# Performance work log

Hardware: AMD Instinct MI355X
Metric: run time of the kernel (lower is better)

The kernel has to match this reference:

```python
import jax, jax.numpy as jnp
from jax import lax
import numpy as np

K_SIZE = 3  # deformable kernel size
PAD = 1
STRIDE = 1


def _conv3x3(x, w, b):
    # plain 3x3 conv, pad 1, stride 1, NCHW/OIHW
    y = lax.conv_general_dilated(x, w, window_strides=(1, 1),
                                 padding=[(1, 1), (1, 1)],
                                 dimension_numbers=('NCHW', 'OIHW', 'NCHW'))
    return y + b[None, :, None, None]


def _deform_sample(x, py, px):
    """Bilinear sample x [B,C,H,W] at float coords py,px [B,K,Ho,Wo].
    Out-of-bounds samples contribute zero (matches torchvision deform_conv2d).
    Returns [B,C,K,Ho,Wo]."""
    B, C, H, W = x.shape
    y0 = jnp.floor(py)
    x0 = jnp.floor(px)
    gat = jax.vmap(lambda img, iy, ix: img[:, iy, ix])  # per-batch gather -> [C,K,Ho,Wo]
    out = jnp.zeros((B, C) + py.shape[1:], dtype=x.dtype)
    for yc, xc in ((y0, x0), (y0, x0 + 1), (y0 + 1, x0), (y0 + 1, x0 + 1)):
        wgt = (1.0 - jnp.abs(py - yc)) * (1.0 - jnp.abs(px - xc))
        valid = (yc >= 0) & (yc <= H - 1) & (xc >= 0) & (xc <= W - 1)
        wgt = jnp.where(valid, wgt, 0.0)
        iy = jnp.clip(yc, 0, H - 1).astype(jnp.int32)
        ix = jnp.clip(xc, 0, W - 1).astype(jnp.int32)
        out = out + wgt[:, None] * gat(x, iy, ix)
    return out


def reference(x, w_off, b_off, w_mask, b_mask, w_dcn, b_dcn):
    k = K_SIZE
    K = k * k
    B, C, H, W = x.shape
    # offset conv (2*K channels: (dy, dx) pairs per kernel position, row-major)
    offset = _conv3x3(x, w_off, b_off)            # [B, 2K, H, W]
    mask = jax.nn.sigmoid(_conv3x3(x, w_mask, b_mask))  # [B, K, H, W]
    off = offset.reshape(B, K, 2, H, W)
    dy, dx = off[:, :, 0], off[:, :, 1]
    ki = (jnp.arange(K) // k).astype(x.dtype)  # kernel row index
    kj = (jnp.arange(K) % k).astype(x.dtype)   # kernel col index
    # sampling coordinates: out position * stride - pad + kernel pos + learned offset
    py = (jnp.arange(H, dtype=x.dtype)[None, None, :, None] * STRIDE - PAD
          + ki[None, :, None, None] + dy)
    px = (jnp.arange(W, dtype=x.dtype)[None, None, None, :] * STRIDE - PAD
          + kj[None, :, None, None] + dx)
    val = _deform_sample(x, py, px) * mask[:, None]   # [B,C,K,H,W]
    Cout = w_dcn.shape[0]
    out = jnp.einsum('ock,bckhw->bohw', w_dcn.reshape(Cout, C, K), val)
    return out + b_dcn[None, :, None, None]


def setup_inputs() -> dict:
    key = jax.random.key(0)
    ks = jax.random.split(key, 6)
    B, C, Cout, H, W, k = 4, 256, 256, 64, 64, 3
    K = k * k
    x = jax.random.normal(ks[0], (B, C, H, W), dtype=jnp.float32)
    # NOTE: original inits offset/mask conv to zeros (degenerate -> plain conv).
    # Use small random weights so offsets/masks are nontrivial but local.
    w_off = jax.random.normal(ks[1], (2 * K, C, 3, 3), dtype=jnp.float32) * 0.01
    b_off = jnp.zeros((2 * K,), dtype=jnp.float32)
    w_mask = jax.random.normal(ks[2], (K, C, 3, 3), dtype=jnp.float32) * 0.01
    b_mask = jnp.zeros((K,), dtype=jnp.float32)
    fan_in = C * K
    w_dcn = jax.random.normal(ks[3], (Cout, C, 3, 3), dtype=jnp.float32) / np.sqrt(fan_in)
    b_dcn = jnp.zeros((Cout,), dtype=jnp.float32)
    return {"x": x, "w_off": w_off, "b_off": b_off, "w_mask": w_mask,
            "b_mask": b_mask, "w_dcn": w_dcn, "b_dcn": b_dcn}
```

## Files before the change

kernel.cpp:

```cpp
#include <hip/hip_runtime.h>
#include <math.h>

#define B_ 4
#define C_ 256
#define CO_ 256
#define H_ 64
#define W_ 64
#define HW_ 4096
#define KK_ 9
#define NCH_ 27

typedef __attribute__((ext_vector_type(8))) short bf16x8;
typedef __attribute__((ext_vector_type(4))) float f32x4;
typedef __attribute__((ext_vector_type(2))) float f32x2;

__device__ inline unsigned short f32_to_bf16(float f) {
    unsigned int u = __float_as_uint(f);
    unsigned int r = (u + 0x7FFFu + ((u >> 16) & 1u)) >> 16;
    return (unsigned short)r;
}

__global__ void prep_all(const float* __restrict__ x, unsigned short* __restrict__ xTh,
                         const float* __restrict__ w_dcn, const float* __restrict__ w_off,
                         const float* __restrict__ w_mask,
                         unsigned short* __restrict__ wTs, unsigned short* __restrict__ wCs) {
    __shared__ float tile[32][33];
    __shared__ float lw[2304];
    const int t = threadIdx.x;
    const int bid = blockIdx.x;
    if (bid < 4096) {
        const int tx = t & 31, ty = t >> 5;
        const int b = bid >> 10;
        const int rem = bid & 1023;
        const int c0 = (rem >> 7) << 5;
        const int hw0 = (rem & 127) << 5;
        const float* xb = x + ((size_t)b << 20);
        unsigned short* xTb = xTh + ((size_t)b << 20);
#pragma unroll
        for (int r = 0; r < 4; ++r) {
            int row = ty + (r << 3);
            tile[row][tx] = xb[((size_t)(c0 + row) << 12) + hw0 + tx];
        }
        __syncthreads();
#pragma unroll
        for (int r = 0; r < 4; ++r) {
            int row = ty + (r << 3);
            xTb[((size_t)(hw0 + row) << 8) + c0 + tx] = f32_to_bf16(tile[tx][row]);
        }
    } else if (bid < 4352) {
        const int o = bid - 4096;
        for (int e = t; e < 2304; e += 256) lw[e] = w_dcn[(size_t)o * 2304 + e];
        __syncthreads();
        for (int e = t; e < 2304; e += 256) {
            int k = e >> 8, c = e & 255;
            int chunk = (k << 2) + (c >> 6), ck = c & 63;
            int pos = (o << 6) + (((ck >> 3) ^ (o & 7)) << 3) + (ck & 7);
            wTs[(size_t)chunk * 16384 + pos] = f32_to_bf16(lw[c * 9 + k]);
        }
    } else {
        const int ch = bid - 4352;
        const float* src = (ch < 18) ? w_off + (size_t)ch * 2304
                         : (ch < NCH_) ? w_mask + (size_t)(ch - 18) * 2304
                         : nullptr;
        for (int e = t; e < 2304; e += 256) lw[e] = src ? src[e] : 0.f;
        __syncthreads();
        for (int e = t; e < 2304; e += 256) {
            int k = e >> 8, c = e & 255;
            int chunk = (k << 2) + (c >> 6), ck = c & 63;
            int pos = (ch << 6) + (((ck >> 3) ^ (ch & 7)) << 3) + (ck & 7);
            wCs[(size_t)chunk * 2048 + pos] = f32_to_bf16(lw[c * 9 + k]);
        }
    }
}

__global__ __launch_bounds__(256, 2) void conv_mfma(
    const unsigned short* __restrict__ xTh, const unsigned short* __restrict__ wCs,
    const float* __restrict__ b_off, const float* __restrict__ b_mask,
    float* __restrict__ offmask) {
    __shared__ alignas(16) unsigned short wlds[3][2048];
    __shared__ alignas(16) unsigned short xlds[3][2048];
    const int t = threadIdx.x;
    const int bid = blockIdx.x;
    const int b = (bid & 7) >> 1;
    const int ph = bid & 1;
    const int hh = bid >> 3;
    const unsigned short* xb = xTh + ((size_t)b << 20);

    auto stage_w = [&](int chunk, int slot) {
        const unsigned short* g = wCs + ((size_t)chunk << 11) + (t << 3);
        __builtin_amdgcn_global_load_lds(
            (const __attribute__((address_space(1))) unsigned int*)g,
            (__attribute__((address_space(3))) unsigned int*)&wlds[slot][t << 3], 16, 0, 0);
    };

    const int xp = t >> 3, xcs = t & 7;
    uint4 xr;
    bool xvalid;
    auto xload = [&](int chunk) {
        int k = chunk >> 2, cc = chunk & 3;
        int ki = k / 3, kj = k % 3;
        int py = hh + ki - 1;
        int px = (ph << 5) + xp + kj - 1;
        xvalid = (py >= 0) & (py < H_) & (px >= 0) & (px < W_);
        int pyc = min(max(py, 0), 63), pxc = min(max(px, 0), 63);
        xr = *(const uint4*)(xb + (((size_t)((pyc << 6) + pxc)) << 8) + (cc << 6) + (xcs << 3));
    };
    auto xwrite = [&](int slot) {
        uint4 u = xvalid ? xr : make_uint4(0u, 0u, 0u, 0u);
        *(uint4*)&xlds[slot][(xp << 6) + ((xcs ^ (xp & 7)) << 3)] = u;
    };

    const int wid = t >> 6, lane = t & 63;
    const int wc = wid >> 1, wp = wid & 1;
    const int m16 = lane & 15, kg = lane >> 4;
    f32x4 acc = {};

    auto compute = [&](int slot) {
#pragma unroll
        for (int ks = 0; ks < 2; ++ks) {
            int s = (ks << 2) + kg;
            int o = (wc << 4) + m16;
            bf16x8 a = *(const bf16x8*)&wlds[slot][(o << 6) + ((s ^ (o & 7)) << 3)];
            int p = (wp << 4) + m16;
            bf16x8 bf = *(const bf16x8*)&xlds[slot][(p << 6) + ((s ^ (p & 7)) << 3)];
            acc = __builtin_amdgcn_mfma_f32_16x16x32_bf16(a, bf, acc, 0, 0, 0);
        }
    };

    xload(0);
    stage_w(0, 0);
    asm volatile("s_waitcnt vmcnt(1)" ::: "memory");
    xwrite(0);

    for (int c = 0; c < 35; ++c) {
        xload(c + 1);
        stage_w(c + 1, (c + 1) % 3);
        asm volatile("s_waitcnt vmcnt(1)" ::: "memory");
        xwrite((c + 1) % 3);
        asm volatile("s_waitcnt lgkmcnt(0)" ::: "memory");
        __builtin_amdgcn_s_barrier();
        asm volatile("" ::: "memory");
        compute(c % 3);
    }
    asm volatile("s_waitcnt vmcnt(0)" ::: "memory");
    asm volatile("s_waitcnt lgkmcnt(0)" ::: "memory");
    __builtin_amdgcn_s_barrier();
    asm volatile("" ::: "memory");
    compute(35 % 3);

    const int pix = (hh << 6) + (ph << 5) + (wp << 4) + m16;
#pragma unroll
    for (int r = 0; r < 4; ++r) {
        int ch = (wc << 4) + (kg << 2) + r;
        if (ch < NCH_) {
            float bias = (ch < 18) ? b_off[ch] : b_mask[ch - 18];
            offmask[(((size_t)b * NCH_ + ch) << 12) + pix] = acc[r] + bias;
        }
    }
}

__global__ __launch_bounds__(512, 4) void dcn_fused(
    const unsigned short* __restrict__ xTh, const float* __restrict__ offmask,
    const unsigned short* __restrict__ wTs, unsigned short* __restrict__ part) {
    __shared__ ushort4 cwh[576];
    __shared__ uchar4 coffb[576];
    __shared__ alignas(16) unsigned short wbuf[2][16384];
    __shared__ alignas(16) unsigned short vbuf[4096];

    const int t = threadIdx.x;
    const int bid = blockIdx.x;
    const int b = (bid & 7) >> 1;
    const int half = bid & 1;
    const int tile64 = bid >> 3;
    const int pix0 = tile64 << 6;
    const unsigned short* xb = xTh + ((size_t)b << 20);
    const float* omb = offmask + (((size_t)b * NCH_) << 12);

    for (int e = t; e < 576; e += 512) {
        int k = e >> 6, p = e & 63;
        int pix = pix0 + p;
        int hh = pix >> 6, ww = pix & 63;
        float dy = omb[((size_t)(2 * k) << 12) + pix];
        float dx = omb[((size_t)(2 * k + 1) << 12) + pix];
        float ml = omb[((size_t)(18 + k) << 12) + pix];
        float m = 1.f / (1.f + __expf(-ml));
        float py = (float)(hh - 1 + (k / 3)) + dy;
        float px = (float)(ww - 1 + (k % 3)) + dx;
        float fy0 = floorf(py), fx0 = floorf(px);
        float ay = py - fy0, ax = px - fx0;
        bool y0v = (fy0 >= 0.f) && (fy0 <= 63.f);
        bool y1v = (fy0 >= -1.f) && (fy0 <= 62.f);
        bool x0v = (fx0 >= 0.f) && (fx0 <= 63.f);
        bool x1v = (fx0 >= -1.f) && (fx0 <= 62.f);
        int y0 = (int)fy0, x0 = (int)fx0;
        int iy0 = min(max(y0, 0), 63), iy1 = min(max(y0 + 1, 0), 63);
        int ix0 = min(max(x0, 0), 63), ix1 = min(max(x0 + 1, 0), 63);
        float w00 = (y0v && x0v) ? m * (1.f - ay) * (1.f - ax) : 0.f;
        float w01 = (y0v && x1v) ? m * (1.f - ay) * ax : 0.f;
        float w10 = (y1v && x0v) ? m * ay * (1.f - ax) : 0.f;
        float w11 = (y1v && x1v) ? m * ay * ax : 0.f;
        cwh[e] = make_ushort4(f32_to_bf16(w00), f32_to_bf16(w01),
                              f32_to_bf16(w10), f32_to_bf16(w11));
        coffb[e] = make_uchar4((unsigned char)iy0, (unsigned char)ix0,
                               (unsigned char)iy1, (unsigned char)ix1);
    }

    const int oct = t & 7, pq = t >> 3;
    const int wid = t >> 6, lane = t & 63;
    const int wo = wid >> 1, wp = wid & 1;
    const int m16 = lane & 15, kg = lane >> 4;
    const int vslot = (pq << 6) + ((oct ^ (pq & 7)) << 3);

    auto stage_w = [&](int c, int slot) {
        int gc = ((c >> 1) << 2) + (half << 1) + (c & 1);
#pragma unroll
        for (int r = 0; r < 4; ++r) {
            int off16 = (r << 9) + t;
            const unsigned short* g = wTs + ((size_t)gc << 14) + (off16 << 3);
            __builtin_amdgcn_global_load_lds(
                (const __attribute__((address_space(1))) unsigned int*)g,
                (__attribute__((address_space(3))) unsigned int*)&wbuf[slot][off16 << 3], 16, 0, 0);
        }
    };

    auto gather = [&](int c, uint4* g) {
        int k = c >> 1, cc = (half << 1) + (c & 1);
        uchar4 q = coffb[(k << 6) + pq];
        const unsigned short* cb = xb + (cc << 6) + (oct << 3);
        g[0] = *(const uint4*)(cb + ((((int)q.x << 6) + q.y) << 8));
        g[1] = *(const uint4*)(cb + ((((int)q.x << 6) + q.w) << 8));
        g[2] = *(const uint4*)(cb + ((((int)q.z << 6) + q.y) << 8));
        g[3] = *(const uint4*)(cb + ((((int)q.z << 6) + q.w) << 8));
    };

    auto finish = [&](int c, const uint4* g) {
        int k = c >> 1;
        ushort4 wv = cwh[(k << 6) + pq];
        float w0 = __uint_as_float((unsigned int)wv.x << 16);
        float w1 = __uint_as_float((unsigned int)wv.y << 16);
        float w2 = __uint_as_float((unsigned int)wv.z << 16);
        float w3 = __uint_as_float((unsigned int)wv.w << 16);
        union { uint4 v; unsigned int u[4]; } A, B2, C2, D2;
        A.v = g[0]; B2.v = g[1]; C2.v = g[2]; D2.v = g[3];
        unsigned int o4[4];
#pragma unroll
        for (int j = 0; j < 4; ++j) {
            f32x2 a2 = {__uint_as_float(A.u[j] << 16),  __uint_as_float(A.u[j] & 0xffff0000u)};
            f32x2 b2 = {__uint_as_float(B2.u[j] << 16), __uint_as_float(B2.u[j] & 0xffff0000u)};
            f32x2 c2 = {__uint_as_float(C2.u[j] << 16), __uint_as_float(C2.u[j] & 0xffff0000u)};
            f32x2 d2 = {__uint_as_float(D2.u[j] << 16), __uint_as_float(D2.u[j] & 0xffff0000u)};
            f32x2 v2 = a2 * w0 + b2 * w1 + c2 * w2 + d2 * w3;
            unsigned int pk;
            asm("v_cvt_pk_bf16_f32 %0, %1, %2" : "=v"(pk) : "v"(v2.x), "v"(v2.y));
            o4[j] = pk;
        }
        *(uint4*)&vbuf[vslot] = make_uint4(o4[0], o4[1], o4[2], o4[3]);
    };

    f32x4 acc[4][2] = {};

    auto compute = [&](int slot) {
#pragma unroll
        for (int ks = 0; ks < 2; ++ks) {
            int s = (ks << 2) + kg;
            bf16x8 aF[4], bF[2];
#pragma unroll
            for (int i = 0; i < 4; ++i) {
                int o = (wo << 6) + (i << 4) + m16;
                aF[i] = *(const bf16x8*)&wbuf[slot][(o << 6) + ((s ^ (o & 7)) << 3)];
            }
#pragma unroll
            for (int j = 0; j < 2; ++j) {
                int p = (wp << 5) + (j << 4) + m16;
                bF[j] = *(const bf16x8*)&vbuf[(p << 6) + ((s ^ (p & 7)) << 3)];
            }
#pragma unroll
            for (int i = 0; i < 4; ++i)
#pragma unroll
                for (int j = 0; j < 2; ++j)
                    acc[i][j] = __builtin_amdgcn_mfma_f32_16x16x32_bf16(
                        aF[i], bF[j], acc[i][j], 0, 0, 0);
        }
    };

    uint4 gA[4], gB[4];

    __syncthreads();
    gather(0, gA);
    stage_w(0, 0);

#define HALFSTEP(CUR, GCUR, GNXT, NW1, NW2)                              \
    __builtin_amdgcn_s_barrier();                                        \
    asm volatile("" ::: "memory");                                       \
    if ((CUR) + 1 < 18) { gather((CUR) + 1, GNXT); stage_w((CUR) + 1, ((CUR) + 1) & 1); } \
    asm volatile("s_waitcnt vmcnt(" #NW1 ")" ::: "memory");              \
    finish((CUR), GCUR);                                                 \
    asm volatile("s_waitcnt vmcnt(" #NW2 ") lgkmcnt(0)" ::: "memory");   \
    __builtin_amdgcn_s_barrier();                                        \
    asm volatile("" ::: "memory");                                       \
    __builtin_amdgcn_s_setprio(1);                                       \
    compute((CUR) & 1);                                                  \
    __builtin_amdgcn_s_setprio(0);

    for (int c = 0; c < 16; c += 2) {
        HALFSTEP(c, gA, gB, 12, 8)
        HALFSTEP(c + 1, gB, gA, 12, 8)
    }
    HALFSTEP(16, gA, gB, 12, 8)
    HALFSTEP(17, gB, gA, 4, 0)
#undef HALFSTEP

    unsigned short* pd = part + (((size_t)((half << 2) + b)) << 20);
#pragma unroll
    for (int i = 0; i < 4; ++i) {
        int ob = (wo << 6) + (i << 4) + (kg << 2);
#pragma unroll
        for (int j = 0; j < 2; ++j) {
            int p = pix0 + (wp << 5) + (j << 4) + m16;
#pragma unroll
            for (int r = 0; r < 4; ++r) {
                int oo = ob + r;
                pd[(((size_t)oo) << 12) + p] = f32_to_bf16(acc[i][j][r]);
            }
        }
    }
}

__global__ __launch_bounds__(256) void combine_out(
    const unsigned short* __restrict__ part, const float* __restrict__ b_dcn,
    float* __restrict__ out) {
    int i = (blockIdx.x * 256 + threadIdx.x) << 3;
    float bias = b_dcn[(i >> 12) & 255];
    union { uint4 v; unsigned int u[4]; } A, B2;
    A.v  = *(const uint4*)(part + i);
    B2.v = *(const uint4*)(part + ((size_t)4 << 20) + i);
    float r[8];
#pragma unroll
    for (int j = 0; j < 4; ++j) {
        float a_lo = __uint_as_float(A.u[j] << 16);
        float a_hi = __uint_as_float(A.u[j] & 0xffff0000u);
        float b_lo = __uint_as_float(B2.u[j] << 16);
        float b_hi = __uint_as_float(B2.u[j] & 0xffff0000u);
        r[2 * j]     = a_lo + b_lo + bias;
        r[2 * j + 1] = a_hi + b_hi + bias;
    }
    *(float4*)(out + i)     = make_float4(r[0], r[1], r[2], r[3]);
    *(float4*)(out + i + 4) = make_float4(r[4], r[5], r[6], r[7]);
}

extern "C" void kernel_launch(void* const* d_in, const int* in_sizes, int n_in,
                              void* d_out, int out_size, void* d_ws, size_t ws_size,
                              hipStream_t stream) {
    const float* x      = (const float*)d_in[0];
    const float* w_off  = (const float*)d_in[1];
    const float* b_off  = (const float*)d_in[2];
    const float* w_mask = (const float*)d_in[3];
    const float* b_mask = (const float*)d_in[4];
    const float* w_dcn  = (const float*)d_in[5];
    const float* b_dcn  = (const float*)d_in[6];
    float* out = (float*)d_out;

    float* ws = (float*)d_ws;
    float* offmask = ws;
    unsigned short* xTh = (unsigned short*)(offmask + (size_t)B_ * NCH_ * HW_);
    unsigned short* wTs = xTh + ((size_t)B_ * HW_ * C_);
    unsigned short* wCs = wTs + (size_t)36 * 16384;
    unsigned short* part = wCs + (size_t)36 * 2048;

    prep_all<<<dim3(4384), dim3(256), 0, stream>>>(x, xTh, w_dcn, w_off, w_mask, wTs, wCs);
    conv_mfma<<<dim3(512), dim3(256), 0, stream>>>(xTh, wCs, b_off, b_mask, offmask);
    dcn_fused<<<dim3(512), dim3(512), 0, stream>>>(xTh, offmask, wTs, part);
    combine_out<<<dim3(2048), dim3(256), 0, stream>>>(part, b_dcn, out);
}
```

Baseline: 72.87 us.

## Fuse split-K combine into DCN kernel via last-arriver atomic flags

Removes the separate combine_out launch. Each dcn_fused block increments a per-(batch,tile) atomic counter after writing its bf16 partial, and the second arriving block sums both halves, adds the bias and writes the fp32 output. Flags are zeroed in prep_all. This saves one kernel launch and a full pass over the partials, at the cost of an atomic, two extra barriers and a tail of combine work in half the blocks. Correctness depends on acquire/release ordering of the partial writes through the agent-scope atomic.

Measured after the change: 90.31 us. 23.9% more time.

```diff
diff --git a/kernel.cpp b/kernel.cpp
--- a/kernel.cpp
+++ b/kernel.cpp
@@ -23,7 +23,8 @@
 __global__ void prep_all(const float* __restrict__ x, unsigned short* __restrict__ xTh,
                          const float* __restrict__ w_dcn, const float* __restrict__ w_off,
                          const float* __restrict__ w_mask,
-                         unsigned short* __restrict__ wTs, unsigned short* __restrict__ wCs) {
+                         unsigned short* __restrict__ wTs, unsigned short* __restrict__ wCs,
+                         unsigned int* __restrict__ flags) {
     __shared__ float tile[32][33];
     __shared__ float lw[2304];
     const int t = threadIdx.x;
@@ -49,6 +50,7 @@
         }
     } else if (bid < 4352) {
         const int o = bid - 4096;
+        if (bid == 4096) flags[t] = 0u;
         for (int e = t; e < 2304; e += 256) lw[e] = w_dcn[(size_t)o * 2304 + e];
         __syncthreads();
         for (int e = t; e < 2304; e += 256) {
@@ -161,11 +163,14 @@
 
 __global__ __launch_bounds__(512, 4) void dcn_fused(
     const unsigned short* __restrict__ xTh, const float* __restrict__ offmask,
-    const unsigned short* __restrict__ wTs, unsigned short* __restrict__ part) {
+    const unsigned short* __restrict__ wTs, unsigned short* __restrict__ part,
+    unsigned int* __restrict__ flags, const float* __restrict__ b_dcn,
+    float* __restrict__ out) {
     __shared__ ushort4 cwh[576];
     __shared__ uchar4 coffb[576];
     __shared__ alignas(16) unsigned short wbuf[2][16384];
     __shared__ alignas(16) unsigned short vbuf[4096];
+    __shared__ unsigned int who;
 
     const int t = threadIdx.x;
     const int bid = blockIdx.x;
@@ -324,28 +329,38 @@
             }
         }
     }
-}
-
-__global__ __launch_bounds__(256) void combine_out(
-    const unsigned short* __restrict__ part, const float* __restrict__ b_dcn,
-    float* __restrict__ out) {
-    int i = (blockIdx.x * 256 + threadIdx.x) << 3;
-    float bias = b_dcn[(i >> 12) & 255];
-    union { uint4 v; unsigned int u[4]; } A, B2;
-    A.v  = *(const uint4*)(part + i);
-    B2.v = *(const uint4*)(part + ((size_t)4 << 20) + i);
-    float r[8];
-#pragma unroll
-    for (int j = 0; j < 4; ++j) {
-        float a_lo = __uint_as_float(A.u[j] << 16);
-        float a_hi = __uint_as_float(A.u[j] & 0xffff0000u);
-        float b_lo = __uint_as_float(B2.u[j] << 16);
-        float b_hi = __uint_as_float(B2.u[j] & 0xffff0000u);
-        r[2 * j]     = a_lo + b_lo + bias;
-        r[2 * j + 1] = a_hi + b_hi + bias;
-    }
-    *(float4*)(out + i)     = make_float4(r[0], r[1], r[2], r[3]);
-    *(float4*)(out + i + 4) = make_float4(r[4], r[5], r[6], r[7]);
+
+    __syncthreads();
+    if (t == 0) {
+        who = __hip_atomic_fetch_add(&flags[(b << 6) | tile64], 1u,
+                                     __ATOMIC_ACQ_REL, __HIP_MEMORY_SCOPE_AGENT);
+    }
+    __syncthreads();
+    if (who == 1u) {
+        const unsigned short* p0 = part + (((size_t)b) << 20);
+        const unsigned short* p1 = part + (((size_t)(4 + b)) << 20);
+        for (int e = t; e < 2048; e += 512) {
+            int o = e >> 3, pg8 = (e & 7) << 3;
+            size_t idx = (((size_t)o) << 12) + pix0 + pg8;
+            float bias = b_dcn[o];
+            union { uint4 v; unsigned int u[4]; } A, B2;
+            A.v  = *(const uint4*)(p0 + idx);
+            B2.v = *(const uint4*)(p1 + idx);
+            float r[8];
+#pragma unroll
+            for (int j = 0; j < 4; ++j) {
+                float a_lo = __uint_as_float(A.u[j] << 16);
+                float a_hi = __uint_as_float(A.u[j] & 0xffff0000u);
+                float b_lo = __uint_as_float(B2.u[j] << 16);
+                float b_hi = __uint_as_float(B2.u[j] & 0xffff0000u);
+                r[2 * j]     = a_lo + b_lo + bias;
+                r[2 * j + 1] = a_hi + b_hi + bias;
+            }
+            float* od = out + (((size_t)(b << 8) + o) << 12) + pix0 + pg8;
+            *(float4*)od       = make_float4(r[0], r[1], r[2], r[3]);
+            *(float4*)(od + 4) = make_float4(r[4], r[5], r[6], r[7]);
+        }
+    }
 }
 
 extern "C" void kernel_launch(void* const* d_in, const int* in_sizes, int n_in,
@@ -366,9 +381,9 @@
     unsigned short* wTs = xTh + ((size_t)B_ * HW_ * C_);
     unsigned short* wCs = wTs + (size_t)36 * 16384;
     unsigned short* part = wCs + (size_t)36 * 2048;
-
-    prep_all<<<dim3(4384), dim3(256), 0, stream>>>(x, xTh, w_dcn, w_off, w_mask, wTs, wCs);
+    unsigned int* flags = (unsigned int*)(part + ((size_t)8 << 20));
+
+    prep_all<<<dim3(4384), dim3(256), 0, stream>>>(x, xTh, w_dcn, w_off, w_mask, wTs, wCs, flags);
     conv_mfma<<<dim3(512), dim3(256), 0, stream>>>(xTh, wCs, b_off, b_mask, offmask);
-    dcn_fused<<<dim3(512), dim3(512), 0, stream>>>(xTh, offmask, wTs, part);
-    combine_out<<<dim3(2048), dim3(256), 0, stream>>>(part, b_dcn, out);
-}
+    dcn_fused<<<dim3(512), dim3(512), 0, stream>>>(xTh, offmask, wTs, part, flags, b_dcn, out);
+}
```
